# Kernel tuning notes

Measured on AMD Instinct MI355X. Metric: run time of the kernel, lower is better.

The kernel has to match this reference:

```python
import jax, jax.numpy as jnp
import numpy as np

N_HEAD = 32
N_QUERY_GROUPS = 8
HEAD_SIZE = 128
N_EMBD = 4096


def apply_rope(x, cos, sin):
    # x: [B, H, T, D]; cos/sin: [T, D] (rotary_percentage = 1.0 so D = head_size)
    d = x.shape[-1]
    x1, x2 = x[..., : d // 2], x[..., d // 2:]
    rotated = jnp.concatenate([-x2, x1], axis=-1)
    return x * cos + rotated * sin


def setup_inputs() -> dict:
    key = jax.random.key(0)
    k1, k2, k3, k4, k5 = jax.random.split(key, 5)
    B, T = 1, 2048
    x = jax.random.normal(k1, (B, T, N_EMBD), dtype=jnp.float32)
    # realistic rope angles
    theta = 10000.0 ** (-jnp.arange(0, HEAD_SIZE // 2, dtype=jnp.float32) * 2.0 / HEAD_SIZE)
    ang = jnp.arange(T, dtype=jnp.float32)[:, None] * theta[None, :]
    ang = jnp.concatenate([ang, ang], axis=-1)  # [T, HEAD_SIZE]
    cos, sin = jnp.cos(ang), jnp.sin(ang)
    qkv_dim = (N_HEAD + 2 * N_QUERY_GROUPS) * HEAD_SIZE  # 6144
    w_attn = jax.random.normal(k2, (qkv_dim, N_EMBD), dtype=jnp.float32) * (N_EMBD ** -0.5)
    w_proj = jax.random.normal(k3, (N_EMBD, N_HEAD * HEAD_SIZE), dtype=jnp.float32) * ((N_HEAD * HEAD_SIZE) ** -0.5)
    return {"x": x, "cos": cos, "sin": sin, "w_attn": w_attn, "w_proj": w_proj}


def reference(x, cos, sin, w_attn, w_proj):
    B, T, C = x.shape
    G, hs = N_QUERY_GROUPS, HEAD_SIZE
    q_per_kv = N_HEAD // G  # 4
    total_qkv = q_per_kv + 2

    qkv = jnp.einsum('btc,oc->bto', x, w_attn)  # [B, T, 6144]
    qkv = qkv.reshape(B, T, G, total_qkv, hs).transpose(0, 2, 3, 1, 4)  # [B, G, total, T, hs]
    q = qkv[:, :, :q_per_kv]              # [B, G, qpk, T, hs]
    k = qkv[:, :, q_per_kv:q_per_kv + 1]  # [B, G, 1,   T, hs]
    v = qkv[:, :, q_per_kv + 1:]          # [B, G, 1,   T, hs]

    # GQA expand to per-query heads, then flatten head dims
    k = jnp.broadcast_to(k, (B, G, q_per_kv, T, hs))
    v = jnp.broadcast_to(v, (B, G, q_per_kv, T, hs))
    q = q.reshape(B, N_HEAD, T, hs)
    k = k.reshape(B, N_HEAD, T, hs)
    v = v.reshape(B, N_HEAD, T, hs)

    # rotary_percentage = 1.0 -> rope over full head dim
    q = apply_rope(q, cos, sin)
    k = apply_rope(k, cos, sin)

    scale = 1.0 / jnp.sqrt(jnp.float32(hs))
    scores = jnp.einsum('bhqd,bhkd->bhqk', q, k) * scale  # [B, H, T, T]
    causal = jnp.tril(jnp.ones((T, T), dtype=bool))
    scores = jnp.where(causal, scores, jnp.finfo(scores.dtype).min)
    attn = jax.nn.softmax(scores, axis=-1)
    y = jnp.einsum('bhqk,bhkd->bhqd', attn, v)  # [B, H, T, hs]
    y = y.transpose(0, 2, 1, 3).reshape(B, T, N_HEAD * hs)
    return jnp.einsum('bto,co->btc', y, w_proj)  # [B, T, C]
```

## Files before the change

kernel.cpp:

```cpp
#include <hip/hip_runtime.h>
#include <hip/hip_bf16.h>

typedef __attribute__((ext_vector_type(8))) short short8;
typedef __attribute__((ext_vector_type(4))) float f32x4;

__device__ inline unsigned short f2bf(float f) {
  __hip_bfloat16 h = __float2bfloat16(f);
  return *reinterpret_cast<unsigned short*>(&h);
}
__device__ inline float bf2f(unsigned short u) {
  union { unsigned u; float f; } v; v.u = ((unsigned)u) << 16;
  return v.f;
}

#define GLOAD_LDS16(g, l)                                          \
  __builtin_amdgcn_global_load_lds(                                \
      (const __attribute__((address_space(1))) void*)(g),          \
      (__attribute__((address_space(3))) void*)(l), 16, 0, 0)

#define MFMA16(a, b, c) __builtin_amdgcn_mfma_f32_16x16x32_bf16((a), (b), (c), 0, 0, 0)

#define LGKM0()                                              \
  asm volatile("s_waitcnt lgkmcnt(0)" ::: "memory");         \
  __builtin_amdgcn_sched_barrier(0);

__global__ void cvt3(const float* __restrict__ x, const float* __restrict__ wa,
                     const float* __restrict__ wp, unsigned short* __restrict__ Xb,
                     unsigned short* __restrict__ Wa, unsigned short* __restrict__ Wp) {
  const int N_X = 1048576, N_WA = 3145728;
  const int TOT = 6291456;
  for (int i = blockIdx.x * 256 + threadIdx.x; i < TOT; i += gridDim.x * 256) {
    const float* src; unsigned short* dst; int off;
    if (i < N_X)            { src = x;  dst = Xb; off = i; }
    else if (i < N_X + N_WA){ src = wa; dst = Wa; off = i - N_X; }
    else                    { src = wp; dst = Wp; off = i - N_X - N_WA; }
    const float4* p = (const float4*)src + (size_t)off * 2;
    float4 a = p[0], b = p[1];
    short8 v;
    v[0] = f2bf(a.x); v[1] = f2bf(a.y); v[2] = f2bf(a.z); v[3] = f2bf(a.w);
    v[4] = f2bf(b.x); v[5] = f2bf(b.y); v[6] = f2bf(b.z); v[7] = f2bf(b.w);
    *((short8*)dst + off) = v;
  }
}

__global__ __launch_bounds__(512, 2)
void gemm_qkv(const unsigned short* __restrict__ A, const unsigned short* __restrict__ B,
              unsigned short* __restrict__ C, int M, int N, int K) {
  __shared__ __align__(16) unsigned short lds[2][448 * 64];
  const int t = threadIdx.x, lane = t & 63, w = t >> 6;
  const int wm = w >> 2, wn = w & 3;
  const int r16 = lane & 15, kg = lane >> 4;
  const int bm = blockIdx.x & 7, bn = blockIdx.x >> 3;
  const int NT = K >> 6;
  const int sr = lane >> 3, sch = lane & 7;
  const unsigned short* Ag = A + (size_t)(bm * 256) * K;
  const unsigned short* Bg = B + (size_t)(bn * 192) * K;

  auto stA = [&](int kt, int j, int b) {
    int rl = j * 64 + w * 8 + sr, sc = sch ^ (rl & 7);
    GLOAD_LDS16(Ag + (size_t)rl * K + kt * 64 + sc * 8, &lds[b][(j * 64 + w * 8) * 64]);
  };
  auto stB = [&](int kt, int j, int b) {
    int rl = j * 64 + w * 8 + sr, sc = sch ^ (rl & 7);
    GLOAD_LDS16(Bg + (size_t)rl * K + kt * 64 + sc * 8, &lds[b][(256 + j * 64 + w * 8) * 64]);
  };
  auto lda = [&](int b, int m, int kk) -> short8 {
    int row = wm * 128 + m * 16 + r16, ch = (kk * 4 + kg) ^ (row & 7);
    return *(const short8*)__builtin_assume_aligned(&lds[b][row * 64 + ch * 8], 16);
  };
  auto ldb = [&](int b, int n, int kk) -> short8 {
    int row = wn * 48 + n * 16 + r16, ch = (kk * 4 + kg) ^ (row & 7);
    return *(const short8*)__builtin_assume_aligned(&lds[b][(256 + row) * 64 + ch * 8], 16);
  };

  f32x4 acc[8][3] = {};
  short8 a0[4][2], a1[4][2], bb[3][2];

#pragma unroll
  for (int j = 0; j < 4; ++j) stA(0, j, 0);
#pragma unroll
  for (int j = 0; j < 3; ++j) stB(0, j, 0);
#pragma unroll
  for (int j = 0; j < 3; ++j) stB(1, j, 1);
  stA(1, 0, 1); stA(1, 2, 1);
  asm volatile("s_waitcnt vmcnt(5)" ::: "memory");
  __builtin_amdgcn_sched_barrier(0);
  __builtin_amdgcn_s_barrier();

  for (int kt = 0; kt < NT; ++kt) {
    const int b = kt & 1;
    const bool pf1 = kt + 1 < NT, pf2 = kt + 2 < NT;

    if (pf1) { stA(kt + 1, 1, b ^ 1); stA(kt + 1, 3, b ^ 1); }
#pragma unroll
    for (int m = 0; m < 4; ++m) { a0[m][0] = lda(b, m, 0); a0[m][1] = lda(b, m, 1); }
#pragma unroll
    for (int n = 0; n < 3; ++n) { bb[n][0] = ldb(b, n, 0); bb[n][1] = ldb(b, n, 1); }
    __builtin_amdgcn_s_barrier();
    LGKM0();
    __builtin_amdgcn_s_setprio(1);
#pragma unroll
    for (int m = 0; m < 4; ++m)
#pragma unroll
      for (int n = 0; n < 3; ++n)
#pragma unroll
        for (int kk = 0; kk < 2; ++kk) acc[m][n] = MFMA16(a0[m][kk], bb[n][kk], acc[m][n]);
    __builtin_amdgcn_s_setprio(0);
    __builtin_amdgcn_s_barrier();

    if (pf2) { stB(kt + 2, 0, b); stB(kt + 2, 1, b); stB(kt + 2, 2, b); stA(kt + 2, 0, b); stA(kt + 2, 2, b); }
#pragma unroll
    for (int m = 0; m < 4; ++m) { a1[m][0] = lda(b, 4 + m, 0); a1[m][1] = lda(b, 4 + m, 1); }
    __builtin_amdgcn_s_barrier();
    LGKM0();
    __builtin_amdgcn_s_setprio(1);
#pragma unroll
    for (int m = 0; m < 4; ++m)
#pragma unroll
      for (int n = 0; n < 3; ++n)
#pragma unroll
        for (int kk = 0; kk < 2; ++kk) acc[4 + m][n] = MFMA16(a1[m][kk], bb[n][kk], acc[4 + m][n]);
    __builtin_amdgcn_s_setprio(0);
    if (pf1) {
      if (pf2) asm volatile("s_waitcnt vmcnt(5)" ::: "memory");
      else     asm volatile("s_waitcnt vmcnt(0)" ::: "memory");
      __builtin_amdgcn_sched_barrier(0);
      __builtin_amdgcn_s_barrier();
    }
  }

#pragma unroll
  for (int m = 0; m < 8; ++m)
#pragma unroll
    for (int n = 0; n < 3; ++n)
#pragma unroll
      for (int j = 0; j < 4; ++j) {
        int row = bm * 256 + wm * 128 + m * 16 + kg * 4 + j;
        int col = bn * 192 + wn * 48 + n * 16 + r16;
        C[(size_t)row * N + col] = f2bf(acc[m][n][j]);
      }
}

__global__ __launch_bounds__(512, 2)
void gemm_proj(const unsigned short* __restrict__ A, const unsigned short* __restrict__ B,
               float* __restrict__ C, int M, int N, int K) {
  __shared__ __align__(16) unsigned short lds[2][384 * 64];
  const int t = threadIdx.x, lane = t & 63, w = t >> 6;
  const int wm = w >> 2, wn = w & 3;
  const int r16 = lane & 15, kg = lane >> 4;
  const int bm = blockIdx.x & 15, bn = blockIdx.x >> 4;
  const int NT = K >> 6;
  const int sr = lane >> 3, sch = lane & 7;
  const unsigned short* Ag = A + (size_t)(bm * 128) * K;
  const unsigned short* Bg = B + (size_t)(bn * 256) * K;

  auto stA = [&](int kt, int j, int b) {
    int rl = j * 64 + w * 8 + sr, sc = sch ^ (rl & 7);
    GLOAD_LDS16(Ag + (size_t)rl * K + kt * 64 + sc * 8, &lds[b][(j * 64 + w * 8) * 64]);
  };
  auto stB = [&](int kt, int j, int b) {
    int rl = j * 64 + w * 8 + sr, sc = sch ^ (rl & 7);
    GLOAD_LDS16(Bg + (size_t)rl * K + kt * 64 + sc * 8, &lds[b][(128 + j * 64 + w * 8) * 64]);
  };
  auto lda = [&](int b, int m, int kk) -> short8 {
    int row = wm * 64 + m * 16 + r16, ch = (kk * 4 + kg) ^ (row & 7);
    return *(const short8*)__builtin_assume_aligned(&lds[b][row * 64 + ch * 8], 16);
  };
  auto ldb = [&](int b, int n, int kk) -> short8 {
    int row = wn * 64 + n * 16 + r16, ch = (kk * 4 + kg) ^ (row & 7);
    return *(const short8*)__builtin_assume_aligned(&lds[b][(128 + row) * 64 + ch * 8], 16);
  };

  f32x4 acc[4][4] = {};
  short8 af[4][2], bb[4][2];

#pragma unroll
  for (int j = 0; j < 2; ++j) stA(0, j, 0);
#pragma unroll
  for (int j = 0; j < 4; ++j) stB(0, j, 0);
#pragma unroll
  for (int j = 0; j < 2; ++j) stA(1, j, 1);
  asm volatile("s_waitcnt vmcnt(2)" ::: "memory");
  __builtin_amdgcn_sched_barrier(0);
  __builtin_amdgcn_s_barrier();

  for (int kt = 0; kt < NT; ++kt) {
    const int b = kt & 1;
    const bool pf1 = kt + 1 < NT, pf2 = kt + 2 < NT;

    if (pf1) { stB(kt + 1, 0, b ^ 1); stB(kt + 1, 1, b ^ 1); stB(kt + 1, 2, b ^ 1); stB(kt + 1, 3, b ^ 1); }
#pragma unroll
    for (int m = 0; m < 4; ++m) { af[m][0] = lda(b, m, 0); af[m][1] = lda(b, m, 1); }
#pragma unroll
    for (int n = 0; n < 2; ++n) { bb[n][0] = ldb(b, n, 0); bb[n][1] = ldb(b, n, 1); }
    __builtin_amdgcn_s_barrier();
    LGKM0();
    __builtin_amdgcn_s_setprio(1);
#pragma unroll
    for (int m = 0; m < 4; ++m)
#pragma unroll
      for (int n = 0; n < 2; ++n)
#pragma unroll
        for (int kk = 0; kk < 2; ++kk) acc[m][n] = MFMA16(af[m][kk], bb[n][kk], acc[m][n]);
    __builtin_amdgcn_s_setprio(0);
    __builtin_amdgcn_s_barrier();

#pragma unroll
    for (int n = 2; n < 4; ++n) { bb[n][0] = ldb(b, n, 0); bb[n][1] = ldb(b, n, 1); }
    if (pf2) { stA(kt + 2, 0, b); stA(kt + 2, 1, b); }
    __builtin_amdgcn_s_barrier();
    LGKM0();
    __builtin_amdgcn_s_setprio(1);
#pragma unroll
    for (int m = 0; m < 4; ++m)
#pragma unroll
      for (int n = 2; n < 4; ++n)
#pragma unroll
        for (int kk = 0; kk < 2; ++kk) acc[m][n] = MFMA16(af[m][kk], bb[n][kk], acc[m][n]);
    __builtin_amdgcn_s_setprio(0);
    if (pf1) {
      if (pf2) asm volatile("s_waitcnt vmcnt(2)" ::: "memory");
      else     asm volatile("s_waitcnt vmcnt(0)" ::: "memory");
      __builtin_amdgcn_sched_barrier(0);
      __builtin_amdgcn_s_barrier();
    }
  }

#pragma unroll
  for (int m = 0; m < 4; ++m)
#pragma unroll
    for (int n = 0; n < 4; ++n)
#pragma unroll
      for (int j = 0; j < 4; ++j) {
        int row = bm * 128 + wm * 64 + m * 16 + kg * 4 + j;
        int col = bn * 256 + wn * 64 + n * 16 + r16;
        C[(size_t)row * N + col] = acc[m][n][j];
      }
}

__global__ void rope_qk(const unsigned short* __restrict__ qkv,
                        const float* __restrict__ cosb, const float* __restrict__ sinb,
                        unsigned short* __restrict__ Q, unsigned short* __restrict__ K) {
  int pair = blockIdx.x * 4 + (threadIdx.x >> 6);
  int l = threadIdx.x & 63;
  int t = pair / 40, slot = pair - t * 40;
  const unsigned short* src;
  unsigned short* dst;
  float scale;
  if (slot < 32) {
    int g = slot >> 2, j = slot & 3;
    src = qkv + (size_t)t * 6144 + g * 768 + j * 128;
    dst = Q + ((size_t)slot * 2048 + t) * 128;
    scale = 0.08838834764831845f;
  } else {
    int g = slot - 32;
    src = qkv + (size_t)t * 6144 + g * 768 + 512;
    dst = K + ((size_t)g * 2048 + t) * 128;
    scale = 1.0f;
  }
  float x1 = bf2f(src[l]), x2 = bf2f(src[64 + l]);
  float c1 = cosb[t * 128 + l], s1 = sinb[t * 128 + l];
  float c2 = cosb[t * 128 + 64 + l], s2 = sinb[t * 128 + 64 + l];
  dst[l]      = f2bf((x1 * c1 - x2 * s1) * scale);
  dst[64 + l] = f2bf((x2 * c2 + x1 * s2) * scale);
}

__global__ void transpose_v(const unsigned short* __restrict__ qkv,
                            unsigned short* __restrict__ Vt) {
  __shared__ __align__(16) unsigned short tile[64][136];
  int g = blockIdx.y, t0 = blockIdx.x * 64;
  int th = threadIdx.x;
  int r = th >> 2, c0 = (th & 3) * 32;
  const unsigned short* src = qkv + (size_t)(t0 + r) * 6144 + g * 768 + 640 + c0;
#pragma unroll
  for (int i = 0; i < 4; ++i)
    *(short8*)&tile[r][c0 + i * 8] = *(const short8*)(src + i * 8);
  __syncthreads();
  int d = th >> 1, tc = (th & 1) * 32;
  unsigned short* dst = Vt + (size_t)(g * 128 + d) * 2048 + t0 + tc;
#pragma unroll
  for (int j = 0; j < 32; ++j) dst[j] = tile[tc + j][d];
}

__global__ __launch_bounds__(256, 2)
void flash_attn(const unsigned short* __restrict__ Q, const unsigned short* __restrict__ K,
                const unsigned short* __restrict__ Vt, unsigned short* __restrict__ Y) {
  __shared__ __align__(16) unsigned short Ksm[2][64 * 128];
  __shared__ __align__(16) unsigned short Vsm[2][128 * 64];

  const int h = blockIdx.y, g = h >> 2;
  const int t = threadIdx.x, lane = t & 63, w = t >> 6;
  const int r16 = lane & 15, kg = lane >> 4;
  const bool odd = kg & 1;
  const bool hi = kg >> 1;
  const bool useswap = odd ^ hi;

  const unsigned short* Kg = K + (size_t)g * 2048 * 128;
  const unsigned short* Vg = Vt + (size_t)g * 128 * 2048;

  const int krl = lane >> 4, kc = lane & 15;
  const int vrl = lane >> 3, vc = lane & 7;

  auto stage = [&](int kvs, int b) {
#pragma unroll
    for (int i = 0; i < 4; ++i) {
      int row = w * 16 + i * 4 + krl;
      int sc = kc ^ (row & 7);
      GLOAD_LDS16(Kg + (size_t)(kvs + row) * 128 + sc * 8,
                  &Ksm[b][(w * 16 + i * 4) * 128]);
    }
#pragma unroll
    for (int i = 0; i < 4; ++i) {
      int d = w * 32 + i * 8 + vrl;
      int sc = vc ^ (d & 7);
      GLOAD_LDS16(Vg + (size_t)d * 2048 + kvs + sc * 8,
                  &Vsm[b][(w * 32 + i * 8) * 64]);
    }
  };

  auto process = [&](int q0) {
    short8 qf[4];
    const unsigned short* qrow = Q + ((size_t)h * 2048 + q0 + w * 16 + r16) * 128;
#pragma unroll
    for (int kk = 0; kk < 4; ++kk) qf[kk] = *(const short8*)(qrow + kk * 32 + kg * 8);

    f32x4 o[8] = {};
    float mrow = -1e30f, lrow = 0.f;
    const int qg = q0 + w * 16 + r16;
    const int nt = q0 / 64 + 1;

    __syncthreads();
    stage(0, 0);

    for (int kt = 0; kt < nt; ++kt) {
      const int b = kt & 1;
      const int kv0 = kt * 64;
      __syncthreads();
      if (kt + 1 < nt) stage((kt + 1) * 64, b ^ 1);

      f32x4 s[4] = {};
      __builtin_amdgcn_s_setprio(1);
#pragma unroll
      for (int n = 0; n < 4; ++n) {
        int kr = n * 16 + r16;
#pragma unroll
        for (int kk = 0; kk < 4; ++kk) {
          short8 kf = *(const short8*)__builtin_assume_aligned(
              &Ksm[b][kr * 128 + ((kk * 32 + kg * 8) ^ ((kr & 7) << 3))], 16);
          s[n] = __builtin_amdgcn_mfma_f32_16x16x32_bf16(kf, qf[kk], s[n], 0, 0, 0);
        }
      }
      __builtin_amdgcn_s_setprio(0);

      if (kv0 + 63 > q0 + w * 16) {
#pragma unroll
        for (int n = 0; n < 4; ++n)
#pragma unroll
          for (int j = 0; j < 4; ++j)
            if (kv0 + n * 16 + kg * 4 + j > qg) s[n][j] = -1e30f;
      }

      float rmax = -1e30f;
#pragma unroll
      for (int n = 0; n < 4; ++n)
#pragma unroll
        for (int j = 0; j < 4; ++j) rmax = fmaxf(rmax, s[n][j]);
      rmax = fmaxf(rmax, __shfl_xor(rmax, 16));
      rmax = fmaxf(rmax, __shfl_xor(rmax, 32));

      if (__builtin_amdgcn_ballot_w64(rmax > mrow)) {
        float mnew = fmaxf(mrow, rmax);
        float fac = __expf(mrow - mnew);
        mrow = mnew;
        lrow *= fac;
        float fj[4];
#pragma unroll
        for (int j = 0; j < 4; ++j) fj[j] = __shfl(fac, kg * 4 + j);
#pragma unroll
        for (int f = 0; f < 8; ++f)
#pragma unroll
          for (int j = 0; j < 4; ++j) o[f][j] *= fj[j];
      }

      float p[4][4];
      float rs = 0.f;
#pragma unroll
      for (int n = 0; n < 4; ++n)
#pragma unroll
        for (int j = 0; j < 4; ++j) {
          p[n][j] = __expf(s[n][j] - mrow);
          rs += p[n][j];
        }
      rs += __shfl_xor(rs, 16);
      rs += __shfl_xor(rs, 32);
      lrow += rs;

      unsigned bpk[4][2], xpk[4][2];
#pragma unroll
      for (int n = 0; n < 4; ++n)
#pragma unroll
        for (int i = 0; i < 2; ++i)
          bpk[n][i] = (unsigned)f2bf(p[n][2 * i]) | ((unsigned)f2bf(p[n][2 * i + 1]) << 16);
#pragma unroll
      for (int n = 0; n < 4; ++n)
#pragma unroll
        for (int i = 0; i < 2; ++i) xpk[n][i] = __shfl_xor(bpk[n][i], 16);

      unsigned pl[4][2], ph[4][2];
#pragma unroll
      for (int n = 0; n < 4; ++n)
#pragma unroll
        for (int i = 0; i < 2; ++i) {
          pl[n][i] = odd ? xpk[n][i] : bpk[n][i];
          ph[n][i] = odd ? bpk[n][i] : xpk[n][i];
        }

      short8 pa[2];
#pragma unroll
      for (int kk = 0; kk < 2; ++kk) {
        unsigned kp0 = hi ? pl[2 * kk + 1][0] : pl[2 * kk][0];
        unsigned kp1 = hi ? pl[2 * kk + 1][1] : pl[2 * kk][1];
        unsigned kp2 = hi ? ph[2 * kk + 1][0] : ph[2 * kk][0];
        unsigned kp3 = hi ? ph[2 * kk + 1][1] : ph[2 * kk][1];
        unsigned sd0 = hi ? pl[2 * kk][0] : pl[2 * kk + 1][0];
        unsigned sd1 = hi ? pl[2 * kk][1] : pl[2 * kk + 1][1];
        unsigned sd2 = hi ? ph[2 * kk][0] : ph[2 * kk + 1][0];
        unsigned sd3 = hi ? ph[2 * kk][1] : ph[2 * kk + 1][1];
        unsigned g0 = __shfl_xor(sd0, 32), g1 = __shfl_xor(sd1, 32);
        unsigned g2 = __shfl_xor(sd2, 32), g3 = __shfl_xor(sd3, 32);
        union { unsigned u[4]; short8 v; } pu;
        pu.u[0] = useswap ? g0 : kp0;
        pu.u[1] = useswap ? g1 : kp1;
        pu.u[2] = useswap ? g2 : kp2;
        pu.u[3] = useswap ? g3 : kp3;
        pa[kk] = pu.v;
      }

      __builtin_amdgcn_s_setprio(1);
#pragma unroll
      for (int kk = 0; kk < 2; ++kk) {
#pragma unroll
        for (int f = 0; f < 8; ++f) {
          int d = f * 16 + r16;
          short8 vf = *(const short8*)__builtin_assume_aligned(
              &Vsm[b][d * 64 + ((kk * 32 + kg * 8) ^ ((d & 7) << 3))], 16);
          o[f] = __builtin_amdgcn_mfma_f32_16x16x32_bf16(pa[kk], vf, o[f], 0, 0, 0);
        }
      }
      __builtin_amdgcn_s_setprio(0);
    }

    float inv = 1.f / lrow;
    float invj[4];
#pragma unroll
    for (int j = 0; j < 4; ++j) invj[j] = __shfl(inv, kg * 4 + j);
#pragma unroll
    for (int j = 0; j < 4; ++j) {
      int row = q0 + w * 16 + kg * 4 + j;
      unsigned short* yr = Y + (size_t)row * 4096 + h * 128;
#pragma unroll
      for (int f = 0; f < 8; ++f) yr[f * 16 + r16] = f2bf(o[f][j] * invj[j]);
    }
  };

  const int pr = blockIdx.x;
  process(pr * 64);
  process((31 - pr) * 64);
}

extern "C" void kernel_launch(void* const* d_in, const int* in_sizes, int n_in,
                              void* d_out, int out_size, void* d_ws, size_t ws_size,
                              hipStream_t stream) {
  const float* x      = (const float*)d_in[0];
  const float* cosb   = (const float*)d_in[1];
  const float* sinb   = (const float*)d_in[2];
  const float* w_attn = (const float*)d_in[3];
  const float* w_proj = (const float*)d_in[4];
  float* out = (float*)d_out;

  char* ws = (char*)d_ws;
  const size_t MB = 1024 * 1024;
  unsigned short* Xb  = (unsigned short*)(ws);
  unsigned short* Wa  = (unsigned short*)(ws + 16 * MB);
  unsigned short* Wp  = (unsigned short*)(ws + 112 * MB);
  unsigned short* Qb  = (unsigned short*)(ws + 32 * MB);
  unsigned short* Kb  = (unsigned short*)(ws + 48 * MB);
  unsigned short* Vt  = (unsigned short*)(ws + 52 * MB);
  unsigned short* qkv = (unsigned short*)(ws + 64 * MB);
  unsigned short* Yb  = (unsigned short*)(ws + 88 * MB);

  cvt3<<<2048, 256, 0, stream>>>(x, w_attn, w_proj, Xb, Wa, Wp);
  gemm_qkv<<<256, 512, 0, stream>>>(Xb, Wa, qkv, 2048, 6144, 4096);
  rope_qk<<<20480, 256, 0, stream>>>(qkv, cosb, sinb, Qb, Kb);
  transpose_v<<<dim3(32, 8), 256, 0, stream>>>(qkv, Vt);
  flash_attn<<<dim3(16, 32), 256, 0, stream>>>(Qb, Kb, Vt, Yb);
  gemm_proj<<<256, 512, 0, stream>>>(Yb, Wp, out, 2048, 4096, 4096);
}
```

Baseline: 314.0 us.

## Enlarge QKV GEMM tile to 256x256 and split GEMM loops into four-phase pipelines

The QKV GEMM tile grows from 256x192 to 256x256, so the grid drops from 256 to 192 blocks, and launch bounds become one block per SIMD-set. Both GEMMs now issue the full next k-tile prefetch in the prologue and restructure each k-step into four MFMA phases, interleaving LDS fragment reads and global-to-LDS prefetches of the tile two steps ahead. The goal is better operand reuse and more overlap of loads with MFMA. The cost is higher register and LDS use per block and lower occupancy. With 192 blocks, the grid may also underfill the 256 CUs.

```diff
diff --git a/kernel.cpp b/kernel.cpp
--- a/kernel.cpp
+++ b/kernel.cpp
@@ -43,10 +43,10 @@
   }
 }
 
-__global__ __launch_bounds__(512, 2)
+__global__ __launch_bounds__(512, 1)
 void gemm_qkv(const unsigned short* __restrict__ A, const unsigned short* __restrict__ B,
               unsigned short* __restrict__ C, int M, int N, int K) {
-  __shared__ __align__(16) unsigned short lds[2][448 * 64];
+  __shared__ __align__(16) unsigned short lds[2][512 * 64];
   const int t = threadIdx.x, lane = t & 63, w = t >> 6;
   const int wm = w >> 2, wn = w & 3;
   const int r16 = lane & 15, kg = lane >> 4;
@@ -54,7 +54,7 @@
   const int NT = K >> 6;
   const int sr = lane >> 3, sch = lane & 7;
   const unsigned short* Ag = A + (size_t)(bm * 256) * K;
-  const unsigned short* Bg = B + (size_t)(bn * 192) * K;
+  const unsigned short* Bg = B + (size_t)(bn * 256) * K;
 
   auto stA = [&](int kt, int j, int b) {
     int rl = j * 64 + w * 8 + sr, sc = sch ^ (rl & 7);
@@ -69,21 +69,22 @@
     return *(const short8*)__builtin_assume_aligned(&lds[b][row * 64 + ch * 8], 16);
   };
   auto ldb = [&](int b, int n, int kk) -> short8 {
-    int row = wn * 48 + n * 16 + r16, ch = (kk * 4 + kg) ^ (row & 7);
+    int row = wn * 64 + n * 16 + r16, ch = (kk * 4 + kg) ^ (row & 7);
     return *(const short8*)__builtin_assume_aligned(&lds[b][(256 + row) * 64 + ch * 8], 16);
   };
 
-  f32x4 acc[8][3] = {};
-  short8 a0[4][2], a1[4][2], bb[3][2];
+  f32x4 acc[8][4] = {};
+  short8 a0[4][2], a1[4][2], bb[4][2];
 
 #pragma unroll
   for (int j = 0; j < 4; ++j) stA(0, j, 0);
 #pragma unroll
-  for (int j = 0; j < 3; ++j) stB(0, j, 0);
-#pragma unroll
-  for (int j = 0; j < 3; ++j) stB(1, j, 1);
-  stA(1, 0, 1); stA(1, 2, 1);
-  asm volatile("s_waitcnt vmcnt(5)" ::: "memory");
+  for (int j = 0; j < 4; ++j) stB(0, j, 0);
+#pragma unroll
+  for (int j = 0; j < 4; ++j) stA(1, j, 1);
+#pragma unroll
+  for (int j = 0; j < 4; ++j) stB(1, j, 1);
+  asm volatile("s_waitcnt vmcnt(8)" ::: "memory");
   __builtin_amdgcn_sched_barrier(0);
   __builtin_amdgcn_s_barrier();
 
@@ -91,38 +92,63 @@
     const int b = kt & 1;
     const bool pf1 = kt + 1 < NT, pf2 = kt + 2 < NT;
 
-    if (pf1) { stA(kt + 1, 1, b ^ 1); stA(kt + 1, 3, b ^ 1); }
 #pragma unroll
     for (int m = 0; m < 4; ++m) { a0[m][0] = lda(b, m, 0); a0[m][1] = lda(b, m, 1); }
 #pragma unroll
-    for (int n = 0; n < 3; ++n) { bb[n][0] = ldb(b, n, 0); bb[n][1] = ldb(b, n, 1); }
+    for (int n = 0; n < 2; ++n) { bb[n][0] = ldb(b, n, 0); bb[n][1] = ldb(b, n, 1); }
     __builtin_amdgcn_s_barrier();
     LGKM0();
     __builtin_amdgcn_s_setprio(1);
 #pragma unroll
     for (int m = 0; m < 4; ++m)
 #pragma unroll
-      for (int n = 0; n < 3; ++n)
+      for (int n = 0; n < 2; ++n)
 #pragma unroll
         for (int kk = 0; kk < 2; ++kk) acc[m][n] = MFMA16(a0[m][kk], bb[n][kk], acc[m][n]);
     __builtin_amdgcn_s_setprio(0);
     __builtin_amdgcn_s_barrier();
 
-    if (pf2) { stB(kt + 2, 0, b); stB(kt + 2, 1, b); stB(kt + 2, 2, b); stA(kt + 2, 0, b); stA(kt + 2, 2, b); }
+#pragma unroll
+    for (int n = 2; n < 4; ++n) { bb[n][0] = ldb(b, n, 0); bb[n][1] = ldb(b, n, 1); }
+    if (pf2) { stA(kt + 2, 0, b); stA(kt + 2, 2, b); }
+    __builtin_amdgcn_s_barrier();
+    LGKM0();
+    __builtin_amdgcn_s_setprio(1);
+#pragma unroll
+    for (int m = 0; m < 4; ++m)
+#pragma unroll
+      for (int n = 2; n < 4; ++n)
+#pragma unroll
+        for (int kk = 0; kk < 2; ++kk) acc[m][n] = MFMA16(a0[m][kk], bb[n][kk], acc[m][n]);
+    __builtin_amdgcn_s_setprio(0);
+    __builtin_amdgcn_s_barrier();
+
 #pragma unroll
     for (int m = 0; m < 4; ++m) { a1[m][0] = lda(b, 4 + m, 0); a1[m][1] = lda(b, 4 + m, 1); }
+    if (pf2) { stB(kt + 2, 0, b); stB(kt + 2, 1, b); }
     __builtin_amdgcn_s_barrier();
     LGKM0();
     __builtin_amdgcn_s_setprio(1);
 #pragma unroll
     for (int m = 0; m < 4; ++m)
 #pragma unroll
-      for (int n = 0; n < 3; ++n)
+      for (int n = 2; n < 4; ++n)
 #pragma unroll
         for (int kk = 0; kk < 2; ++kk) acc[4 + m][n] = MFMA16(a1[m][kk], bb[n][kk], acc[4 + m][n]);
     __builtin_amdgcn_s_setprio(0);
+    __builtin_amdgcn_s_barrier();
+
+    if (pf2) { stB(kt + 2, 2, b); stB(kt + 2, 3, b); stA(kt + 2, 1, b); stA(kt + 2, 3, b); }
+    __builtin_amdgcn_s_setprio(1);
+#pragma unroll
+    for (int m = 0; m < 4; ++m)
+#pragma unroll
+      for (int n = 0; n < 2; ++n)
+#pragma unroll
+        for (int kk = 0; kk < 2; ++kk) acc[4 + m][n] = MFMA16(a1[m][kk], bb[n][kk], acc[4 + m][n]);
+    __builtin_amdgcn_s_setprio(0);
     if (pf1) {
-      if (pf2) asm volatile("s_waitcnt vmcnt(5)" ::: "memory");
+      if (pf2) asm volatile("s_waitcnt vmcnt(8)" ::: "memory");
       else     asm volatile("s_waitcnt vmcnt(0)" ::: "memory");
       __builtin_amdgcn_sched_barrier(0);
       __builtin_amdgcn_s_barrier();
@@ -132,16 +158,16 @@
 #pragma unroll
   for (int m = 0; m < 8; ++m)
 #pragma unroll
-    for (int n = 0; n < 3; ++n)
+    for (int n = 0; n < 4; ++n)
 #pragma unroll
       for (int j = 0; j < 4; ++j) {
         int row = bm * 256 + wm * 128 + m * 16 + kg * 4 + j;
-        int col = bn * 192 + wn * 48 + n * 16 + r16;
+        int col = bn * 256 + wn * 64 + n * 16 + r16;
         C[(size_t)row * N + col] = f2bf(acc[m][n][j]);
       }
 }
 
-__global__ __launch_bounds__(512, 2)
+__global__ __launch_bounds__(512, 1)
 void gemm_proj(const unsigned short* __restrict__ A, const unsigned short* __restrict__ B,
                float* __restrict__ C, int M, int N, int K) {
   __shared__ __align__(16) unsigned short lds[2][384 * 64];
@@ -180,7 +206,9 @@
   for (int j = 0; j < 4; ++j) stB(0, j, 0);
 #pragma unroll
   for (int j = 0; j < 2; ++j) stA(1, j, 1);
-  asm volatile("s_waitcnt vmcnt(2)" ::: "memory");
+#pragma unroll
+  for (int j = 0; j < 4; ++j) stB(1, j, 1);
+  asm volatile("s_waitcnt vmcnt(6)" ::: "memory");
   __builtin_amdgcn_sched_barrier(0);
   __builtin_amdgcn_s_barrier();
 
@@ -188,16 +216,15 @@
     const int b = kt & 1;
     const bool pf1 = kt + 1 < NT, pf2 = kt + 2 < NT;
 
-    if (pf1) { stB(kt + 1, 0, b ^ 1); stB(kt + 1, 1, b ^ 1); stB(kt + 1, 2, b ^ 1); stB(kt + 1, 3, b ^ 1); }
-#pragma unroll
-    for (int m = 0; m < 4; ++m) { af[m][0] = lda(b, m, 0); af[m][1] = lda(b, m, 1); }
+#pragma unroll
+    for (int m = 0; m < 2; ++m) { af[m][0] = lda(b, m, 0); af[m][1] = lda(b, m, 1); }
 #pragma unroll
     for (int n = 0; n < 2; ++n) { bb[n][0] = ldb(b, n, 0); bb[n][1] = ldb(b, n, 1); }
     __builtin_amdgcn_s_barrier();
     LGKM0();
     __builtin_amdgcn_s_setprio(1);
 #pragma unroll
-    for (int m = 0; m < 4; ++m)
+    for (int m = 0; m < 2; ++m)
 #pragma unroll
       for (int n = 0; n < 2; ++n)
 #pragma unroll
@@ -207,19 +234,44 @@
 
 #pragma unroll
     for (int n = 2; n < 4; ++n) { bb[n][0] = ldb(b, n, 0); bb[n][1] = ldb(b, n, 1); }
+    __builtin_amdgcn_s_barrier();
+    LGKM0();
+    __builtin_amdgcn_s_setprio(1);
+#pragma unroll
+    for (int m = 0; m < 2; ++m)
+#pragma unroll
+      for (int n = 2; n < 4; ++n)
+#pragma unroll
+        for (int kk = 0; kk < 2; ++kk) acc[m][n] = MFMA16(af[m][kk], bb[n][kk], acc[m][n]);
+    __builtin_amdgcn_s_setprio(0);
+    __builtin_amdgcn_s_barrier();
+
+#pragma unroll
+    for (int m = 2; m < 4; ++m) { af[m][0] = lda(b, m, 0); af[m][1] = lda(b, m, 1); }
+    if (pf2) { stB(kt + 2, 0, b); stB(kt + 2, 1, b); stB(kt + 2, 2, b); stB(kt + 2, 3, b); }
+    __builtin_amdgcn_s_barrier();
+    LGKM0();
+    __builtin_amdgcn_s_setprio(1);
+#pragma unroll
+    for (int m = 2; m < 4; ++m)
+#pragma unroll
+      for (int n = 2; n < 4; ++n)
+#pragma unroll
+        for (int kk = 0; kk < 2; ++kk) acc[m][n] = MFMA16(af[m][kk], bb[n][kk], acc[m][n]);
+    __builtin_amdgcn_s_setprio(0);
+    __builtin_amdgcn_s_barrier();
+
     if (pf2) { stA(kt + 2, 0, b); stA(kt + 2, 1, b); }
-    __builtin_amdgcn_s_barrier();
-    LGKM0();
-    __builtin_amdgcn_s_setprio(1);
-#pragma unroll
-    for (int m = 0; m < 4; ++m)
-#pragma unroll
-      for (int n = 2; n < 4; ++n)
+    __builtin_amdgcn_s_setprio(1);
+#pragma unroll
+    for (int m = 2; m < 4; ++m)
+#pragma unroll
+      for (int n = 0; n < 2; ++n)
 #pragma unroll
         for (int kk = 0; kk < 2; ++kk) acc[m][n] = MFMA16(af[m][kk], bb[n][kk], acc[m][n]);
     __builtin_amdgcn_s_setprio(0);
     if (pf1) {
-      if (pf2) asm volatile("s_waitcnt vmcnt(2)" ::: "memory");
+      if (pf2) asm volatile("s_waitcnt vmcnt(6)" ::: "memory");
       else     asm volatile("s_waitcnt vmcnt(0)" ::: "memory");
       __builtin_amdgcn_sched_barrier(0);
       __builtin_amdgcn_s_barrier();
@@ -490,7 +542,7 @@
   unsigned short* Yb  = (unsigned short*)(ws + 88 * MB);
 
   cvt3<<<2048, 256, 0, stream>>>(x, w_attn, w_proj, Xb, Wa, Wp);
-  gemm_qkv<<<256, 512, 0, stream>>>(Xb, Wa, qkv, 2048, 6144, 4096);
+  gemm_qkv<<<192, 512, 0, stream>>>(Xb, Wa, qkv, 2048, 6144, 4096);
   rope_qk<<<20480, 256, 0, stream>>>(qkv, cosb, sinb, Qb, Kb);
   transpose_v<<<dim3(32, 8), 256, 0, stream>>>(qkv, Vt);
   flash_attn<<<dim3(16, 32), 256, 0, stream>>>(Qb, Kb, Vt, Yb);
```

Result: slower. 333.4 us (+6.1%).

## Fuse fp32-to-bf16 weight conversion into GEMM B-operand loads

Applied to the files above, without the earlier changes.

Drops the separate conversion pass over both weight matrices. The GEMMs now read fp32 weights straight into registers, convert them to bf16 and write the swizzled result to LDS inside the pipelined K loop, while x is still converted by a small standalone kernel. This removes a full write and read of the bf16 weight copies. In exchange each GEMM tile reads twice as many bytes per weight and spends VALU and LDS-store work on conversion. Launch bounds drop to one block per CU, likely because register pressure rises.

```diff
diff --git a/kernel.cpp b/kernel.cpp
--- a/kernel.cpp
+++ b/kernel.cpp
@@ -24,27 +24,18 @@
   asm volatile("s_waitcnt lgkmcnt(0)" ::: "memory");         \
   __builtin_amdgcn_sched_barrier(0);
 
-__global__ void cvt3(const float* __restrict__ x, const float* __restrict__ wa,
-                     const float* __restrict__ wp, unsigned short* __restrict__ Xb,
-                     unsigned short* __restrict__ Wa, unsigned short* __restrict__ Wp) {
-  const int N_X = 1048576, N_WA = 3145728;
-  const int TOT = 6291456;
-  for (int i = blockIdx.x * 256 + threadIdx.x; i < TOT; i += gridDim.x * 256) {
-    const float* src; unsigned short* dst; int off;
-    if (i < N_X)            { src = x;  dst = Xb; off = i; }
-    else if (i < N_X + N_WA){ src = wa; dst = Wa; off = i - N_X; }
-    else                    { src = wp; dst = Wp; off = i - N_X - N_WA; }
-    const float4* p = (const float4*)src + (size_t)off * 2;
-    float4 a = p[0], b = p[1];
-    short8 v;
-    v[0] = f2bf(a.x); v[1] = f2bf(a.y); v[2] = f2bf(a.z); v[3] = f2bf(a.w);
-    v[4] = f2bf(b.x); v[5] = f2bf(b.y); v[6] = f2bf(b.z); v[7] = f2bf(b.w);
-    *((short8*)dst + off) = v;
-  }
-}
-
-__global__ __launch_bounds__(512, 2)
-void gemm_qkv(const unsigned short* __restrict__ A, const unsigned short* __restrict__ B,
+__global__ void cvt_x(const float* __restrict__ in, unsigned short* __restrict__ out) {
+  int i = blockIdx.x * 256 + threadIdx.x;
+  const float4* p = (const float4*)in + (size_t)i * 2;
+  float4 a = p[0], b = p[1];
+  short8 v;
+  v[0] = f2bf(a.x); v[1] = f2bf(a.y); v[2] = f2bf(a.z); v[3] = f2bf(a.w);
+  v[4] = f2bf(b.x); v[5] = f2bf(b.y); v[6] = f2bf(b.z); v[7] = f2bf(b.w);
+  *((short8*)out + i) = v;
+}
+
+__global__ __launch_bounds__(512, 1)
+void gemm_qkv(const unsigned short* __restrict__ A, const float* __restrict__ B,
               unsigned short* __restrict__ C, int M, int N, int K) {
   __shared__ __align__(16) unsigned short lds[2][448 * 64];
   const int t = threadIdx.x, lane = t & 63, w = t >> 6;
@@ -54,15 +45,31 @@
   const int NT = K >> 6;
   const int sr = lane >> 3, sch = lane & 7;
   const unsigned short* Ag = A + (size_t)(bm * 256) * K;
-  const unsigned short* Bg = B + (size_t)(bn * 192) * K;
+  const float* Bg = B + (size_t)(bn * 192) * K;
 
   auto stA = [&](int kt, int j, int b) {
     int rl = j * 64 + w * 8 + sr, sc = sch ^ (rl & 7);
     GLOAD_LDS16(Ag + (size_t)rl * K + kt * 64 + sc * 8, &lds[b][(j * 64 + w * 8) * 64]);
   };
-  auto stB = [&](int kt, int j, int b) {
-    int rl = j * 64 + w * 8 + sr, sc = sch ^ (rl & 7);
-    GLOAD_LDS16(Bg + (size_t)rl * K + kt * 64 + sc * 8, &lds[b][(256 + j * 64 + w * 8) * 64]);
+  float4 bu[3], bv[3];
+  auto loadB = [&](int kt) {
+#pragma unroll
+    for (int i = 0; i < 3; ++i) {
+      int ct = t + i * 512, rl = ct >> 3, ch = ct & 7;
+      const float* s = Bg + (size_t)rl * K + kt * 64 + ch * 8;
+      bu[i] = *(const float4*)s; bv[i] = *(const float4*)(s + 4);
+    }
+  };
+  auto writeB = [&](int bb) {
+#pragma unroll
+    for (int i = 0; i < 3; ++i) {
+      int ct = t + i * 512, rl = ct >> 3, ch = ct & 7;
+      int sw = ch ^ (rl & 7);
+      short8 sv;
+      sv[0] = f2bf(bu[i].x); sv[1] = f2bf(bu[i].y); sv[2] = f2bf(bu[i].z); sv[3] = f2bf(bu[i].w);
+      sv[4] = f2bf(bv[i].x); sv[5] = f2bf(bv[i].y); sv[6] = f2bf(bv[i].z); sv[7] = f2bf(bv[i].w);
+      *(short8*)__builtin_assume_aligned(&lds[bb][(256 + rl) * 64 + sw * 8], 16) = sv;
+    }
   };
   auto lda = [&](int b, int m, int kk) -> short8 {
     int row = wm * 128 + m * 16 + r16, ch = (kk * 4 + kg) ^ (row & 7);
@@ -78,12 +85,11 @@
 
 #pragma unroll
   for (int j = 0; j < 4; ++j) stA(0, j, 0);
-#pragma unroll
-  for (int j = 0; j < 3; ++j) stB(0, j, 0);
-#pragma unroll
-  for (int j = 0; j < 3; ++j) stB(1, j, 1);
+  loadB(0);
   stA(1, 0, 1); stA(1, 2, 1);
-  asm volatile("s_waitcnt vmcnt(5)" ::: "memory");
+  writeB(0);
+  LGKM0();
+  asm volatile("s_waitcnt vmcnt(2)" ::: "memory");
   __builtin_amdgcn_sched_barrier(0);
   __builtin_amdgcn_s_barrier();
 
@@ -91,7 +97,7 @@
     const int b = kt & 1;
     const bool pf1 = kt + 1 < NT, pf2 = kt + 2 < NT;
 
-    if (pf1) { stA(kt + 1, 1, b ^ 1); stA(kt + 1, 3, b ^ 1); }
+    if (pf1) { stA(kt + 1, 1, b ^ 1); stA(kt + 1, 3, b ^ 1); loadB(kt + 1); }
 #pragma unroll
     for (int m = 0; m < 4; ++m) { a0[m][0] = lda(b, m, 0); a0[m][1] = lda(b, m, 1); }
 #pragma unroll
@@ -108,7 +114,8 @@
     __builtin_amdgcn_s_setprio(0);
     __builtin_amdgcn_s_barrier();
 
-    if (pf2) { stB(kt + 2, 0, b); stB(kt + 2, 1, b); stB(kt + 2, 2, b); stA(kt + 2, 0, b); stA(kt + 2, 2, b); }
+    if (pf2) { stA(kt + 2, 0, b); stA(kt + 2, 2, b); }
+    if (pf1) writeB(b ^ 1);
 #pragma unroll
     for (int m = 0; m < 4; ++m) { a1[m][0] = lda(b, 4 + m, 0); a1[m][1] = lda(b, 4 + m, 1); }
     __builtin_amdgcn_s_barrier();
@@ -122,7 +129,7 @@
         for (int kk = 0; kk < 2; ++kk) acc[4 + m][n] = MFMA16(a1[m][kk], bb[n][kk], acc[4 + m][n]);
     __builtin_amdgcn_s_setprio(0);
     if (pf1) {
-      if (pf2) asm volatile("s_waitcnt vmcnt(5)" ::: "memory");
+      if (pf2) asm volatile("s_waitcnt vmcnt(2)" ::: "memory");
       else     asm volatile("s_waitcnt vmcnt(0)" ::: "memory");
       __builtin_amdgcn_sched_barrier(0);
       __builtin_amdgcn_s_barrier();
@@ -141,8 +148,8 @@
       }
 }
 
-__global__ __launch_bounds__(512, 2)
-void gemm_proj(const unsigned short* __restrict__ A, const unsigned short* __restrict__ B,
+__global__ __launch_bounds__(512, 1)
+void gemm_proj(const unsigned short* __restrict__ A, const float* __restrict__ B,
                float* __restrict__ C, int M, int N, int K) {
   __shared__ __align__(16) unsigned short lds[2][384 * 64];
   const int t = threadIdx.x, lane = t & 63, w = t >> 6;
@@ -152,15 +159,31 @@
   const int NT = K >> 6;
   const int sr = lane >> 3, sch = lane & 7;
   const unsigned short* Ag = A + (size_t)(bm * 128) * K;
-  const unsigned short* Bg = B + (size_t)(bn * 256) * K;
+  const float* Bg = B + (size_t)(bn * 256) * K;
 
   auto stA = [&](int kt, int j, int b) {
     int rl = j * 64 + w * 8 + sr, sc = sch ^ (rl & 7);
     GLOAD_LDS16(Ag + (size_t)rl * K + kt * 64 + sc * 8, &lds[b][(j * 64 + w * 8) * 64]);
   };
-  auto stB = [&](int kt, int j, int b) {
-    int rl = j * 64 + w * 8 + sr, sc = sch ^ (rl & 7);
-    GLOAD_LDS16(Bg + (size_t)rl * K + kt * 64 + sc * 8, &lds[b][(128 + j * 64 + w * 8) * 64]);
+  float4 bu[4], bv[4];
+  auto loadB = [&](int kt) {
+#pragma unroll
+    for (int i = 0; i < 4; ++i) {
+      int ct = t + i * 512, rl = ct >> 3, ch = ct & 7;
+      const float* s = Bg + (size_t)rl * K + kt * 64 + ch * 8;
+      bu[i] = *(const float4*)s; bv[i] = *(const float4*)(s + 4);
+    }
+  };
+  auto writeB = [&](int bb) {
+#pragma unroll
+    for (int i = 0; i < 4; ++i) {
+      int ct = t + i * 512, rl = ct >> 3, ch = ct & 7;
+      int sw = ch ^ (rl & 7);
+      short8 sv;
+      sv[0] = f2bf(bu[i].x); sv[1] = f2bf(bu[i].y); sv[2] = f2bf(bu[i].z); sv[3] = f2bf(bu[i].w);
+      sv[4] = f2bf(bv[i].x); sv[5] = f2bf(bv[i].y); sv[6] = f2bf(bv[i].z); sv[7] = f2bf(bv[i].w);
+      *(short8*)__builtin_assume_aligned(&lds[bb][(128 + rl) * 64 + sw * 8], 16) = sv;
+    }
   };
   auto lda = [&](int b, int m, int kk) -> short8 {
     int row = wm * 64 + m * 16 + r16, ch = (kk * 4 + kg) ^ (row & 7);
@@ -174,12 +197,11 @@
   f32x4 acc[4][4] = {};
   short8 af[4][2], bb[4][2];
 
-#pragma unroll
-  for (int j = 0; j < 2; ++j) stA(0, j, 0);
-#pragma unroll
-  for (int j = 0; j < 4; ++j) stB(0, j, 0);
-#pragma unroll
-  for (int j = 0; j < 2; ++j) stA(1, j, 1);
+  stA(0, 0, 0); stA(0, 1, 0);
+  loadB(0);
+  stA(1, 0, 1); stA(1, 1, 1);
+  writeB(0);
+  LGKM0();
   asm volatile("s_waitcnt vmcnt(2)" ::: "memory");
   __builtin_amdgcn_sched_barrier(0);
   __builtin_amdgcn_s_barrier();
@@ -188,7 +210,7 @@
     const int b = kt & 1;
     const bool pf1 = kt + 1 < NT, pf2 = kt + 2 < NT;
 
-    if (pf1) { stB(kt + 1, 0, b ^ 1); stB(kt + 1, 1, b ^ 1); stB(kt + 1, 2, b ^ 1); stB(kt + 1, 3, b ^ 1); }
+    if (pf1) loadB(kt + 1);
 #pragma unroll
     for (int m = 0; m < 4; ++m) { af[m][0] = lda(b, m, 0); af[m][1] = lda(b, m, 1); }
 #pragma unroll
@@ -205,9 +227,10 @@
     __builtin_amdgcn_s_setprio(0);
     __builtin_amdgcn_s_barrier();
 
+    if (pf2) { stA(kt + 2, 0, b); stA(kt + 2, 1, b); }
+    if (pf1) writeB(b ^ 1);
 #pragma unroll
     for (int n = 2; n < 4; ++n) { bb[n][0] = ldb(b, n, 0); bb[n][1] = ldb(b, n, 1); }
-    if (pf2) { stA(kt + 2, 0, b); stA(kt + 2, 1, b); }
     __builtin_amdgcn_s_barrier();
     LGKM0();
     __builtin_amdgcn_s_setprio(1);
@@ -481,18 +504,16 @@
   char* ws = (char*)d_ws;
   const size_t MB = 1024 * 1024;
   unsigned short* Xb  = (unsigned short*)(ws);
-  unsigned short* Wa  = (unsigned short*)(ws + 16 * MB);
-  unsigned short* Wp  = (unsigned short*)(ws + 112 * MB);
   unsigned short* Qb  = (unsigned short*)(ws + 32 * MB);
   unsigned short* Kb  = (unsigned short*)(ws + 48 * MB);
   unsigned short* Vt  = (unsigned short*)(ws + 52 * MB);
   unsigned short* qkv = (unsigned short*)(ws + 64 * MB);
   unsigned short* Yb  = (unsigned short*)(ws + 88 * MB);
 
-  cvt3<<<2048, 256, 0, stream>>>(x, w_attn, w_proj, Xb, Wa, Wp);
-  gemm_qkv<<<256, 512, 0, stream>>>(Xb, Wa, qkv, 2048, 6144, 4096);
+  cvt_x<<<4096, 256, 0, stream>>>(x, Xb);
+  gemm_qkv<<<256, 512, 0, stream>>>(Xb, w_attn, qkv, 2048, 6144, 4096);
   rope_qk<<<20480, 256, 0, stream>>>(qkv, cosb, sinb, Qb, Kb);
   transpose_v<<<dim3(32, 8), 256, 0, stream>>>(qkv, Vt);
   flash_attn<<<dim3(16, 32), 256, 0, stream>>>(Qb, Kb, Vt, Yb);
-  gemm_proj<<<256, 512, 0, stream>>>(Yb, Wp, out, 2048, 4096, 4096);
-}
+  gemm_proj<<<256, 512, 0, stream>>>(Yb, w_proj, out, 2048, 4096, 4096);
+}
```

After: 402.9 us. 28.3% more time.

## Restructure proj GEMM into four-phase pipeline and merge rope with V transpose

Applied to the files above, without the earlier changes.

The projection GEMM loop is split into four MFMA quadrant phases. B-tile prefetch now runs two stages ahead, alongside the A prefetch, with the vmcnt waits updated to match, and launch bounds drop to one block per CU. Separately, the rope and V-transpose kernels are fused into a single launch that branches on block index, removing one kernel launch. The deeper prefetch is meant to hide global-load latency better. In exchange it adds barriers and gives up the two-blocks-per-CU occupancy hint.

```diff
diff --git a/kernel.cpp b/kernel.cpp
--- a/kernel.cpp
+++ b/kernel.cpp
@@ -141,7 +141,7 @@
       }
 }
 
-__global__ __launch_bounds__(512, 2)
+__global__ __launch_bounds__(512, 1)
 void gemm_proj(const unsigned short* __restrict__ A, const unsigned short* __restrict__ B,
                float* __restrict__ C, int M, int N, int K) {
   __shared__ __align__(16) unsigned short lds[2][384 * 64];
@@ -180,7 +180,9 @@
   for (int j = 0; j < 4; ++j) stB(0, j, 0);
 #pragma unroll
   for (int j = 0; j < 2; ++j) stA(1, j, 1);
-  asm volatile("s_waitcnt vmcnt(2)" ::: "memory");
+#pragma unroll
+  for (int j = 0; j < 4; ++j) stB(1, j, 1);
+  asm volatile("s_waitcnt vmcnt(6)" ::: "memory");
   __builtin_amdgcn_sched_barrier(0);
   __builtin_amdgcn_s_barrier();
 
@@ -188,16 +190,15 @@
     const int b = kt & 1;
     const bool pf1 = kt + 1 < NT, pf2 = kt + 2 < NT;
 
-    if (pf1) { stB(kt + 1, 0, b ^ 1); stB(kt + 1, 1, b ^ 1); stB(kt + 1, 2, b ^ 1); stB(kt + 1, 3, b ^ 1); }
-#pragma unroll
-    for (int m = 0; m < 4; ++m) { af[m][0] = lda(b, m, 0); af[m][1] = lda(b, m, 1); }
+#pragma unroll
+    for (int m = 0; m < 2; ++m) { af[m][0] = lda(b, m, 0); af[m][1] = lda(b, m, 1); }
 #pragma unroll
     for (int n = 0; n < 2; ++n) { bb[n][0] = ldb(b, n, 0); bb[n][1] = ldb(b, n, 1); }
     __builtin_amdgcn_s_barrier();
     LGKM0();
     __builtin_amdgcn_s_setprio(1);
 #pragma unroll
-    for (int m = 0; m < 4; ++m)
+    for (int m = 0; m < 2; ++m)
 #pragma unroll
       for (int n = 0; n < 2; ++n)
 #pragma unroll
@@ -207,19 +208,44 @@
 
 #pragma unroll
     for (int n = 2; n < 4; ++n) { bb[n][0] = ldb(b, n, 0); bb[n][1] = ldb(b, n, 1); }
-    if (pf2) { stA(kt + 2, 0, b); stA(kt + 2, 1, b); }
     __builtin_amdgcn_s_barrier();
     LGKM0();
     __builtin_amdgcn_s_setprio(1);
 #pragma unroll
-    for (int m = 0; m < 4; ++m)
+    for (int m = 0; m < 2; ++m)
 #pragma unroll
       for (int n = 2; n < 4; ++n)
+#pragma unroll
+        for (int kk = 0; kk < 2; ++kk) acc[m][n] = MFMA16(af[m][kk], bb[n][kk], acc[m][n]);
+    __builtin_amdgcn_s_setprio(0);
+    __builtin_amdgcn_s_barrier();
+
+#pragma unroll
+    for (int m = 2; m < 4; ++m) { af[m][0] = lda(b, m, 0); af[m][1] = lda(b, m, 1); }
+    if (pf2) { stB(kt + 2, 0, b); stB(kt + 2, 1, b); stB(kt + 2, 2, b); stB(kt + 2, 3, b); }
+    __builtin_amdgcn_s_barrier();
+    LGKM0();
+    __builtin_amdgcn_s_setprio(1);
+#pragma unroll
+    for (int m = 2; m < 4; ++m)
+#pragma unroll
+      for (int n = 2; n < 4; ++n)
+#pragma unroll
+        for (int kk = 0; kk < 2; ++kk) acc[m][n] = MFMA16(af[m][kk], bb[n][kk], acc[m][n]);
+    __builtin_amdgcn_s_setprio(0);
+    __builtin_amdgcn_s_barrier();
+
+    if (pf2) { stA(kt + 2, 0, b); stA(kt + 2, 1, b); }
+    __builtin_amdgcn_s_setprio(1);
+#pragma unroll
+    for (int m = 2; m < 4; ++m)
+#pragma unroll
+      for (int n = 0; n < 2; ++n)
 #pragma unroll
         for (int kk = 0; kk < 2; ++kk) acc[m][n] = MFMA16(af[m][kk], bb[n][kk], acc[m][n]);
     __builtin_amdgcn_s_setprio(0);
     if (pf1) {
-      if (pf2) asm volatile("s_waitcnt vmcnt(2)" ::: "memory");
+      if (pf2) asm volatile("s_waitcnt vmcnt(6)" ::: "memory");
       else     asm volatile("s_waitcnt vmcnt(0)" ::: "memory");
       __builtin_amdgcn_sched_barrier(0);
       __builtin_amdgcn_s_barrier();
@@ -238,48 +264,50 @@
       }
 }
 
-__global__ void rope_qk(const unsigned short* __restrict__ qkv,
+__global__ void rope_tv(const unsigned short* __restrict__ qkv,
                         const float* __restrict__ cosb, const float* __restrict__ sinb,
-                        unsigned short* __restrict__ Q, unsigned short* __restrict__ K) {
-  int pair = blockIdx.x * 4 + (threadIdx.x >> 6);
-  int l = threadIdx.x & 63;
-  int t = pair / 40, slot = pair - t * 40;
-  const unsigned short* src;
-  unsigned short* dst;
-  float scale;
-  if (slot < 32) {
-    int g = slot >> 2, j = slot & 3;
-    src = qkv + (size_t)t * 6144 + g * 768 + j * 128;
-    dst = Q + ((size_t)slot * 2048 + t) * 128;
-    scale = 0.08838834764831845f;
+                        unsigned short* __restrict__ Q, unsigned short* __restrict__ K,
+                        unsigned short* __restrict__ Vt) {
+  __shared__ __align__(16) unsigned short tile[64][136];
+  const int bid = blockIdx.x;
+  if (bid < 20480) {
+    int pair = bid * 4 + (threadIdx.x >> 6);
+    int l = threadIdx.x & 63;
+    int t = pair / 40, slot = pair - t * 40;
+    const unsigned short* src;
+    unsigned short* dst;
+    float scale;
+    if (slot < 32) {
+      int g = slot >> 2, j = slot & 3;
+      src = qkv + (size_t)t * 6144 + g * 768 + j * 128;
+      dst = Q + ((size_t)slot * 2048 + t) * 128;
+      scale = 0.08838834764831845f;
+    } else {
+      int g = slot - 32;
+      src = qkv + (size_t)t * 6144 + g * 768 + 512;
+      dst = K + ((size_t)g * 2048 + t) * 128;
+      scale = 1.0f;
+    }
+    float x1 = bf2f(src[l]), x2 = bf2f(src[64 + l]);
+    float c1 = cosb[t * 128 + l], s1 = sinb[t * 128 + l];
+    float c2 = cosb[t * 128 + 64 + l], s2 = sinb[t * 128 + 64 + l];
+    dst[l]      = f2bf((x1 * c1 - x2 * s1) * scale);
+    dst[64 + l] = f2bf((x2 * c2 + x1 * s2) * scale);
   } else {
-    int g = slot - 32;
-    src = qkv + (size_t)t * 6144 + g * 768 + 512;
-    dst = K + ((size_t)g * 2048 + t) * 128;
-    scale = 1.0f;
+    int b2 = bid - 20480;
+    int g = b2 >> 5, t0 = (b2 & 31) * 64;
+    int th = threadIdx.x;
+    int r = th >> 2, c0 = (th & 3) * 32;
+    const unsigned short* src = qkv + (size_t)(t0 + r) * 6144 + g * 768 + 640 + c0;
+#pragma unroll
+    for (int i = 0; i < 4; ++i)
+      *(short8*)&tile[r][c0 + i * 8] = *(const short8*)(src + i * 8);
+    __syncthreads();
+    int d = th >> 1, tc = (th & 1) * 32;
+    unsigned short* dst = Vt + (size_t)(g * 128 + d) * 2048 + t0 + tc;
+#pragma unroll
+    for (int j = 0; j < 32; ++j) dst[j] = tile[tc + j][d];
   }
-  float x1 = bf2f(src[l]), x2 = bf2f(src[64 + l]);
-  float c1 = cosb[t * 128 + l], s1 = sinb[t * 128 + l];
-  float c2 = cosb[t * 128 + 64 + l], s2 = sinb[t * 128 + 64 + l];
-  dst[l]      = f2bf((x1 * c1 - x2 * s1) * scale);
-  dst[64 + l] = f2bf((x2 * c2 + x1 * s2) * scale);
-}
-
-__global__ void transpose_v(const unsigned short* __restrict__ qkv,
-                            unsigned short* __restrict__ Vt) {
-  __shared__ __align__(16) unsigned short tile[64][136];
-  int g = blockIdx.y, t0 = blockIdx.x * 64;
-  int th = threadIdx.x;
-  int r = th >> 2, c0 = (th & 3) * 32;
-  const unsigned short* src = qkv + (size_t)(t0 + r) * 6144 + g * 768 + 640 + c0;
-#pragma unroll
-  for (int i = 0; i < 4; ++i)
-    *(short8*)&tile[r][c0 + i * 8] = *(const short8*)(src + i * 8);
-  __syncthreads();
-  int d = th >> 1, tc = (th & 1) * 32;
-  unsigned short* dst = Vt + (size_t)(g * 128 + d) * 2048 + t0 + tc;
-#pragma unroll
-  for (int j = 0; j < 32; ++j) dst[j] = tile[tc + j][d];
 }
 
 __global__ __launch_bounds__(256, 2)
@@ -491,8 +519,7 @@
 
   cvt3<<<2048, 256, 0, stream>>>(x, w_attn, w_proj, Xb, Wa, Wp);
   gemm_qkv<<<256, 512, 0, stream>>>(Xb, Wa, qkv, 2048, 6144, 4096);
-  rope_qk<<<20480, 256, 0, stream>>>(qkv, cosb, sinb, Qb, Kb);
-  transpose_v<<<dim3(32, 8), 256, 0, stream>>>(qkv, Vt);
+  rope_tv<<<20736, 256, 0, stream>>>(qkv, cosb, sinb, Qb, Kb, Vt);
   flash_attn<<<dim3(16, 32), 256, 0, stream>>>(Qb, Kb, Vt, Yb);
   gemm_proj<<<256, 512, 0, stream>>>(Yb, Wp, out, 2048, 4096, 4096);
 }
```

Measured after the change: 316.0 us. No clear change (+0.6%).
